# Kernel optimization log

Measured on AMD Instinct MI355X. Metric: run time of the kernel, lower is better.

Reference implementation:

```python
import jax, jax.numpy as jnp
import numpy as np

C = 256
CQK = C // 8  # 32

def setup_inputs() -> dict:
    key = jax.random.key(0)
    ks = jax.random.split(key, 8)
    B, W, H = 4, 64, 64
    s = 0.02
    x = jax.random.normal(ks[0], (B, C, W, H), dtype=jnp.float32)
    Wq = jax.random.normal(ks[1], (CQK, C), dtype=jnp.float32) * s
    bq = jnp.zeros((CQK,), dtype=jnp.float32)
    Wk = jax.random.normal(ks[2], (CQK, C), dtype=jnp.float32) * s
    bk = jnp.zeros((CQK,), dtype=jnp.float32)
    Wv = jax.random.normal(ks[3], (C, C), dtype=jnp.float32) * s
    bv = jnp.zeros((C,), dtype=jnp.float32)
    gamma = jnp.ones((1,), dtype=jnp.float32)  # nonzero so attention path matters
    return {"x": x, "Wq": Wq, "bq": bq, "Wk": Wk, "bk": bk, "Wv": Wv, "bv": bv, "gamma": gamma}

def reference(x, Wq, bq, Wk, bk, Wv, bv, gamma):
    B, Cc, W, H = x.shape
    N = W * H
    xf = x.reshape(B, Cc, N)  # B, C, N (flattened spatial)
    # 1x1 convs == channel-wise linear maps
    q = jnp.einsum('dc,bcn->bnd', Wq, xf) + bq[None, None, :]   # B, N, CQK
    k = jnp.einsum('dc,bcn->bdn', Wk, xf) + bk[None, :, None]   # B, CQK, N
    v = jnp.einsum('dc,bcn->bdn', Wv, xf) + bv[None, :, None]   # B, C, N
    energy = jnp.einsum('bnd,bdm->bnm', q, k)                   # B, N, N (unscaled)
    attention = jax.nn.softmax(energy, axis=-1)
    # out[:, :, i] = sum_j v[:, :, j] * attention[i, j]
    out = jnp.einsum('bdm,bnm->bdn', v, attention)              # B, C, N
    out = out.reshape(B, Cc, W, H)
    return gamma[0] * out + x
```

## Files before the change

kernel.cpp:

```cpp
#include <hip/hip_runtime.h>


#define CB  256
#define DQK 32
#define NN  4096
#define NB  4

typedef __attribute__((ext_vector_type(8))) short  short8;
typedef __attribute__((ext_vector_type(4))) float  f32x4;
typedef __attribute__((ext_vector_type(4))) unsigned short ushort4v;

__device__ inline unsigned short f2bf(float f) {
    union { float f; unsigned u; } cv; cv.f = f;
    unsigned u = cv.u;
    u += 0x7fffu + ((u >> 16) & 1u);
    return (unsigned short)(u >> 16);
}

__device__ inline float fast_exp2(float x) {
    float r;
    asm("v_exp_f32 %0, %1" : "=v"(r) : "v"(x));
    return r;
}

__device__ inline void gl16(const unsigned short* g, unsigned short* l) {
    __builtin_amdgcn_global_load_lds(
        (const __attribute__((address_space(1))) unsigned int*)g,
        (__attribute__((address_space(3))) unsigned int*)l, 16, 0, 0);
}

__device__ inline float bcast_row(const float* s, int lane) {
    int n = lane & 15;
    int src = (n >> 2) << 4;
    float b0 = __shfl(s[0], src, 64);
    float b1 = __shfl(s[1], src, 64);
    float b2 = __shfl(s[2], src, 64);
    float b3 = __shfl(s[3], src, 64);
    float r01 = (n & 1) ? b1 : b0;
    float r23 = (n & 1) ? b3 : b2;
    return (n & 2) ? r23 : r01;
}

__global__ __launch_bounds__(256) void proj_mfma(
    const float* __restrict__ x,
    const float* __restrict__ Wq, const float* __restrict__ bq,
    const float* __restrict__ Wk, const float* __restrict__ bk,
    const float* __restrict__ Wv, const float* __restrict__ bv,
    unsigned short* __restrict__ qo,
    unsigned short* __restrict__ ko,
    unsigned short* __restrict__ vo)
{
    __shared__ unsigned short ws[64 * 256];
    __shared__ unsigned short xs[64 * 256];

    const int bid = blockIdx.x;
    const int nb  = bid / 5;
    const int mg  = bid % 5;
    const int b   = nb >> 6;
    const int n0  = (nb & 63) << 6;
    const int t   = threadIdx.x;
    const int w   = t >> 6;
    const int lane = t & 63;

    {
        const int row = t >> 2;
        const int q4  = t & 3;
        const float* wsrc;
        if (mg < 4) wsrc = Wv + (size_t)(mg * 64 + row) * CB;
        else        wsrc = (row < 32) ? (Wq + (size_t)row * CB)
                                      : (Wk + (size_t)(row - 32) * CB);
        #pragma unroll
        for (int o = 0; o < 8; ++o) {
            int c = q4 * 64 + o * 8;
            f32x4 a0 = *(const f32x4*)(wsrc + c);
            f32x4 a1 = *(const f32x4*)(wsrc + c + 4);
            short8 pk;
            pk[0]=(short)f2bf(a0[0]); pk[1]=(short)f2bf(a0[1]);
            pk[2]=(short)f2bf(a0[2]); pk[3]=(short)f2bf(a0[3]);
            pk[4]=(short)f2bf(a1[0]); pk[5]=(short)f2bf(a1[1]);
            pk[6]=(short)f2bf(a1[2]); pk[7]=(short)f2bf(a1[3]);
            *(short8*)((char*)ws + row * 512 + ((c * 2) ^ ((row & 7) << 4))) = pk;
        }
    }
    {
        const float* xb = x + (size_t)b * CB * NN + n0;
        #pragma unroll
        for (int o = 0; o < 8; ++o) {
            int c0 = w * 64 + o * 8;
            float tf[8];
            #pragma unroll
            for (int i = 0; i < 8; ++i)
                tf[i] = xb[(size_t)(c0 + i) * NN + lane];
            short8 pk;
            #pragma unroll
            for (int i = 0; i < 8; ++i) pk[i] = (short)f2bf(tf[i]);
            *(short8*)((char*)xs + lane * 512 + ((c0 * 2) ^ ((lane & 7) << 4))) = pk;
        }
    }
    __syncthreads();

    const int l15 = lane & 15, l4 = lane >> 4;
    f32x4 acc[4];
    #pragma unroll
    for (int i = 0; i < 4; ++i) acc[i] = (f32x4){0.f, 0.f, 0.f, 0.f};

    #pragma unroll
    for (int kk = 0; kk < 8; ++kk) {
        int kb = kk * 64 + l4 * 16;
        int mrow = w * 16 + l15;
        short8 af = *(const short8*)((char*)ws + mrow * 512 + (kb ^ ((l15 & 7) << 4)));
        #pragma unroll
        for (int nf = 0; nf < 4; ++nf) {
            int n = nf * 16 + l15;
            short8 bfr = *(const short8*)((char*)xs + n * 512 + (kb ^ ((l15 & 7) << 4)));
            acc[nf] = __builtin_amdgcn_mfma_f32_16x16x32_bf16(af, bfr, acc[nf], 0, 0, 0);
        }
    }

    if (mg < 4) {
        #pragma unroll
        for (int nf = 0; nf < 4; ++nf) {
            #pragma unroll
            for (int r = 0; r < 4; ++r) {
                int m = mg * 64 + w * 16 + l4 * 4 + r;
                float val = acc[nf][r] + bv[m];
                vo[((size_t)b * CB + m) * NN + n0 + nf * 16 + l15] = f2bf(val);
            }
        }
    } else {
        const int dl = w * 16 + l4 * 4;
        #pragma unroll
        for (int nf = 0; nf < 4; ++nf) {
            size_t n = (size_t)b * NN + n0 + nf * 16 + l15;
            ushort4v pk;
            if (dl < 32) {
                #pragma unroll
                for (int r = 0; r < 4; ++r) pk[r] = f2bf(acc[nf][r] + bq[dl + r]);
                *(ushort4v*)(qo + n * DQK + dl) = pk;
            } else {
                #pragma unroll
                for (int r = 0; r < 4; ++r) pk[r] = f2bf(acc[nf][r] + bk[dl - 32 + r]);
                *(ushort4v*)(ko + n * DQK + dl - 32) = pk;
            }
        }
    }
}

__global__ __launch_bounds__(512, 4) void attn_kernel(
    const unsigned short* __restrict__ q,
    const unsigned short* __restrict__ k,
    const unsigned short* __restrict__ v,
    const float* __restrict__ x,
    const float* __restrict__ gamma,
    float* __restrict__ out)
{
    __shared__ unsigned short ksl[64 * 32];
    __shared__ unsigned short vsl[128 * 64];
    __shared__ unsigned short plds[8][1024];

    const int bid = blockIdx.x;
    const int swz = (bid & 7) * 64 + (bid >> 3);
    const int dh = swz & 1;
    const int nt = (swz >> 1) & 63;
    const int b  = swz >> 7;
    const int n0 = nt << 6;
    const int d0 = dh << 7;

    const int t    = threadIdx.x;
    const int w    = t >> 6;
    const int lane = t & 63;
    const int l15  = lane & 15;
    const int l4   = lane >> 4;
    const int qg   = w & 3;
    const int dsub = w >> 2;

    const unsigned short* qb = q + ((size_t)b * NN + n0 + qg * 16) * DQK;
    short8 qf = *(const short8*)(qb + (size_t)l15 * DQK + l4 * 8);

    f32x4 acc[4];
    #pragma unroll
    for (int i = 0; i < 4; ++i) acc[i] = (f32x4){0.f, 0.f, 0.f, 0.f};
    float psum[4] = {0.f, 0.f, 0.f, 0.f};

    const unsigned short* kb = k + (size_t)b * NN * DQK;
    const unsigned short* vb = v + (size_t)b * CB * NN;
    unsigned short* myp = plds[w];
    const float L2E = 1.44269504088896f;
    const f32x4 zero4 = {0.f, 0.f, 0.f, 0.f};

    const int krow = (w << 4) + (lane >> 2);
    const int kso  = (lane & 3) ^ ((lane >> 2) & 3);
    const int vso  = (lane & 7) ^ (lane >> 3);
    const int vrow0 = (w << 4) + (lane >> 3);
    const int vrow1 = vrow0 + 8;

    for (int m0 = 0; m0 < NN; m0 += 64) {
        __syncthreads();
        if (w < 4)
            gl16(kb + (size_t)(m0 + krow) * DQK + kso * 8, &ksl[w * 512]);
        gl16(vb + (size_t)(d0 + vrow0) * NN + m0 + vso * 8, &vsl[(w * 2 + 0) * 512]);
        gl16(vb + (size_t)(d0 + vrow1) * NN + m0 + vso * 8, &vsl[(w * 2 + 1) * 512]);
        asm volatile("s_waitcnt vmcnt(0)" ::: "memory");
        __syncthreads();

        f32x4 sf[4];
        #pragma unroll
        for (int mt = 0; mt < 4; ++mt) {
            int row  = mt * 16 + l15;
            int slot = l4 ^ (l15 & 3);
            short8 kf = *(const short8*)(&ksl[row * 32 + slot * 8]);
            sf[mt] = __builtin_amdgcn_mfma_f32_16x16x32_bf16(qf, kf, zero4, 0, 0, 0);
        }

        f32x4 pvv[4];
        #pragma unroll
        for (int r = 0; r < 4; ++r) {
            float p0 = fast_exp2(sf[0][r] * L2E);
            float p1 = fast_exp2(sf[1][r] * L2E);
            float p2 = fast_exp2(sf[2][r] * L2E);
            float p3 = fast_exp2(sf[3][r] * L2E);
            pvv[0][r] = p0; pvv[1][r] = p1; pvv[2][r] = p2; pvv[3][r] = p3;
            psum[r] += (p0 + p1) + (p2 + p3);
        }

        #pragma unroll
        for (int mt = 0; mt < 4; ++mt) {
            #pragma unroll
            for (int r = 0; r < 4; ++r) {
                int row = l4 * 4 + r;
                int col = mt * 16 + l15;
                int off = row * 128 + ((col * 2) ^ ((row & 7) << 4));
                myp[off >> 1] = f2bf(pvv[mt][r]);
            }
        }
        asm volatile("s_waitcnt lgkmcnt(0)" ::: "memory");
        __builtin_amdgcn_sched_barrier(0);

        short8 pb0, pb1;
        {
            int base = l15 * 128;
            int sw   = (l15 & 7) << 4;
            pb0 = *(const short8*)(myp + ((base + ((l4 * 16)      ^ sw)) >> 1));
            pb1 = *(const short8*)(myp + ((base + ((64 + l4 * 16) ^ sw)) >> 1));
        }

        #pragma unroll
        for (int dt = 0; dt < 4; ++dt) {
            int row = dsub * 64 + dt * 16 + l15;
            int s0  = (l4)     ^ (l15 & 7);
            int s1  = (4 + l4) ^ (l15 & 7);
            short8 vf0 = *(const short8*)(&vsl[row * 64 + s0 * 8]);
            short8 vf1 = *(const short8*)(&vsl[row * 64 + s1 * 8]);
            acc[dt] = __builtin_amdgcn_mfma_f32_16x16x32_bf16(vf0, pb0, acc[dt], 0, 0, 0);
            acc[dt] = __builtin_amdgcn_mfma_f32_16x16x32_bf16(vf1, pb1, acc[dt], 0, 0, 0);
        }
    }

    float runs[4];
    #pragma unroll
    for (int r = 0; r < 4; ++r) {
        float s = psum[r];
        s += __shfl_xor(s, 1); s += __shfl_xor(s, 2);
        s += __shfl_xor(s, 4); s += __shfl_xor(s, 8);
        runs[r] = s;
    }

    float rs  = bcast_row(runs, lane);
    float inv = 1.0f / rs;
    float g   = gamma[0];
    const size_t xoff = ((size_t)b * CB + d0 + dsub * 64) * NN + n0 + qg * 16;
    const float* xb = x + xoff;
    float*       ob = out + xoff;
    #pragma unroll
    for (int dt = 0; dt < 4; ++dt) {
        #pragma unroll
        for (int r = 0; r < 4; ++r) {
            size_t o = (size_t)(dt * 16 + l4 * 4 + r) * NN + l15;
            ob[o] = g * acc[dt][r] * inv + xb[o];
        }
    }
}

extern "C" void kernel_launch(void* const* d_in, const int* in_sizes, int n_in,
                              void* d_out, int out_size, void* d_ws, size_t ws_size,
                              hipStream_t stream) {
    const float* x     = (const float*)d_in[0];
    const float* Wq    = (const float*)d_in[1];
    const float* bq    = (const float*)d_in[2];
    const float* Wk    = (const float*)d_in[3];
    const float* bk    = (const float*)d_in[4];
    const float* Wv    = (const float*)d_in[5];
    const float* bv    = (const float*)d_in[6];
    const float* gamma = (const float*)d_in[7];
    float* out = (float*)d_out;

    unsigned short* qs = (unsigned short*)d_ws;
    unsigned short* ks = qs + (size_t)NB * NN * DQK;
    unsigned short* vs = ks + (size_t)NB * NN * DQK;

    proj_mfma<<<5 * NB * (NN / 64), 256, 0, stream>>>(x, Wq, bq, Wk, bk, Wv, bv, qs, ks, vs);
    attn_kernel<<<NB * (NN / 64) * 2, 512, 0, stream>>>(qs, ks, vs, x, gamma, out);
}
```

Baseline: 188.2 us.

## Double-buffer K/V tiles and fold log2e scale into Q projection

Attention kernel now stages K and V tiles into two LDS buffers so the next tile's global loads overlap the current tile's QK, softmax and PV MFMAs, with one barrier per iteration. The QK MFMA operands are swapped so scores come out transposed, which allows packed bf16 conversion and vectorized P stores, and reduces the final row-sum to two shuffles. The log2(e) factor is folded into Wq/bq in the projection kernel to remove a multiply per exp. This doubles K/V LDS usage, which may lower occupancy.

```diff
diff --git a/kernel.cpp b/kernel.cpp
--- a/kernel.cpp
+++ b/kernel.cpp
@@ -9,6 +9,9 @@
 typedef __attribute__((ext_vector_type(8))) short  short8;
 typedef __attribute__((ext_vector_type(4))) float  f32x4;
 typedef __attribute__((ext_vector_type(4))) unsigned short ushort4v;
+typedef __attribute__((ext_vector_type(2))) unsigned int   uint2v;
+
+#define L2E 1.44269504088896f
 
 __device__ inline unsigned short f2bf(float f) {
     union { float f; unsigned u; } cv; cv.f = f;
@@ -23,22 +26,16 @@
     return r;
 }
 
+__device__ inline unsigned int cvtpk(float lo, float hi) {
+    unsigned int r;
+    asm("v_cvt_pk_bf16_f32 %0, %1, %2" : "=v"(r) : "v"(lo), "v"(hi));
+    return r;
+}
+
 __device__ inline void gl16(const unsigned short* g, unsigned short* l) {
     __builtin_amdgcn_global_load_lds(
         (const __attribute__((address_space(1))) unsigned int*)g,
         (__attribute__((address_space(3))) unsigned int*)l, 16, 0, 0);
-}
-
-__device__ inline float bcast_row(const float* s, int lane) {
-    int n = lane & 15;
-    int src = (n >> 2) << 4;
-    float b0 = __shfl(s[0], src, 64);
-    float b1 = __shfl(s[1], src, 64);
-    float b2 = __shfl(s[2], src, 64);
-    float b3 = __shfl(s[3], src, 64);
-    float r01 = (n & 1) ? b1 : b0;
-    float r23 = (n & 1) ? b3 : b2;
-    return (n & 2) ? r23 : r01;
 }
 
 __global__ __launch_bounds__(256) void proj_mfma(
@@ -66,19 +63,20 @@
         const int row = t >> 2;
         const int q4  = t & 3;
         const float* wsrc;
+        float scale = 1.0f;
         if (mg < 4) wsrc = Wv + (size_t)(mg * 64 + row) * CB;
-        else        wsrc = (row < 32) ? (Wq + (size_t)row * CB)
-                                      : (Wk + (size_t)(row - 32) * CB);
+        else if (row < 32) { wsrc = Wq + (size_t)row * CB; scale = L2E; }
+        else               wsrc = Wk + (size_t)(row - 32) * CB;
         #pragma unroll
         for (int o = 0; o < 8; ++o) {
             int c = q4 * 64 + o * 8;
             f32x4 a0 = *(const f32x4*)(wsrc + c);
             f32x4 a1 = *(const f32x4*)(wsrc + c + 4);
             short8 pk;
-            pk[0]=(short)f2bf(a0[0]); pk[1]=(short)f2bf(a0[1]);
-            pk[2]=(short)f2bf(a0[2]); pk[3]=(short)f2bf(a0[3]);
-            pk[4]=(short)f2bf(a1[0]); pk[5]=(short)f2bf(a1[1]);
-            pk[6]=(short)f2bf(a1[2]); pk[7]=(short)f2bf(a1[3]);
+            pk[0]=(short)f2bf(a0[0]*scale); pk[1]=(short)f2bf(a0[1]*scale);
+            pk[2]=(short)f2bf(a0[2]*scale); pk[3]=(short)f2bf(a0[3]*scale);
+            pk[4]=(short)f2bf(a1[0]*scale); pk[5]=(short)f2bf(a1[1]*scale);
+            pk[6]=(short)f2bf(a1[2]*scale); pk[7]=(short)f2bf(a1[3]*scale);
             *(short8*)((char*)ws + row * 512 + ((c * 2) ^ ((row & 7) << 4))) = pk;
         }
     }
@@ -135,7 +133,7 @@
             ushort4v pk;
             if (dl < 32) {
                 #pragma unroll
-                for (int r = 0; r < 4; ++r) pk[r] = f2bf(acc[nf][r] + bq[dl + r]);
+                for (int r = 0; r < 4; ++r) pk[r] = f2bf(acc[nf][r] + bq[dl + r] * L2E);
                 *(ushort4v*)(qo + n * DQK + dl) = pk;
             } else {
                 #pragma unroll
@@ -154,8 +152,8 @@
     const float* __restrict__ gamma,
     float* __restrict__ out)
 {
-    __shared__ unsigned short ksl[64 * 32];
-    __shared__ unsigned short vsl[128 * 64];
+    __shared__ unsigned short ksl[2][64 * 32];
+    __shared__ unsigned short vsl[2][128 * 64];
     __shared__ unsigned short plds[8][1024];
 
     const int bid = blockIdx.x;
@@ -180,58 +178,67 @@
     f32x4 acc[4];
     #pragma unroll
     for (int i = 0; i < 4; ++i) acc[i] = (f32x4){0.f, 0.f, 0.f, 0.f};
-    float psum[4] = {0.f, 0.f, 0.f, 0.f};
+    float psum = 0.f;
 
     const unsigned short* kb = k + (size_t)b * NN * DQK;
     const unsigned short* vb = v + (size_t)b * CB * NN;
     unsigned short* myp = plds[w];
-    const float L2E = 1.44269504088896f;
     const f32x4 zero4 = {0.f, 0.f, 0.f, 0.f};
 
     const int krow = (w << 4) + (lane >> 2);
-    const int kso  = (lane & 3) ^ ((lane >> 2) & 3);
+    const int kso  = (lane & 3) ^ ((lane >> 2) & 3) ^ ((lane >> 4) & 3);
     const int vso  = (lane & 7) ^ (lane >> 3);
     const int vrow0 = (w << 4) + (lane >> 3);
     const int vrow1 = vrow0 + 8;
 
-    for (int m0 = 0; m0 < NN; m0 += 64) {
-        __syncthreads();
-        if (w < 4)
-            gl16(kb + (size_t)(m0 + krow) * DQK + kso * 8, &ksl[w * 512]);
-        gl16(vb + (size_t)(d0 + vrow0) * NN + m0 + vso * 8, &vsl[(w * 2 + 0) * 512]);
-        gl16(vb + (size_t)(d0 + vrow1) * NN + m0 + vso * 8, &vsl[(w * 2 + 1) * 512]);
-        asm volatile("s_waitcnt vmcnt(0)" ::: "memory");
-        __syncthreads();
+    const int kslot = (l4 ^ (l15 & 3) ^ ((l15 >> 2) & 3)) * 8;
+    const int vs0 = ((l4)     ^ (l15 & 7)) * 8;
+    const int vs1 = ((l4 + 4) ^ (l15 & 7)) * 8;
+    const int psw = (l15 & 7) << 4;
+
+    #define STAGE(buf, m0)                                                        \
+        do {                                                                      \
+            if (w < 4)                                                            \
+                gl16(kb + (size_t)((m0) + krow) * DQK + kso * 8, &ksl[buf][w * 512]); \
+            gl16(vb + (size_t)(d0 + vrow0) * NN + (m0) + vso * 8,                 \
+                 &vsl[buf][(w * 2 + 0) * 512]);                                   \
+            gl16(vb + (size_t)(d0 + vrow1) * NN + (m0) + vso * 8,                 \
+                 &vsl[buf][(w * 2 + 1) * 512]);                                   \
+        } while (0)
+
+    STAGE(0, 0);
+    __syncthreads();
+
+    for (int it = 0; it < 64; ++it) {
+        const int cur = it & 1;
+        if (it < 63) STAGE(cur ^ 1, (it + 1) * 64);
+
+        const unsigned short* kc = ksl[cur];
+        const unsigned short* vc = vsl[cur];
 
         f32x4 sf[4];
         #pragma unroll
         for (int mt = 0; mt < 4; ++mt) {
-            int row  = mt * 16 + l15;
-            int slot = l4 ^ (l15 & 3);
-            short8 kf = *(const short8*)(&ksl[row * 32 + slot * 8]);
-            sf[mt] = __builtin_amdgcn_mfma_f32_16x16x32_bf16(qf, kf, zero4, 0, 0, 0);
-        }
-
-        f32x4 pvv[4];
-        #pragma unroll
-        for (int r = 0; r < 4; ++r) {
-            float p0 = fast_exp2(sf[0][r] * L2E);
-            float p1 = fast_exp2(sf[1][r] * L2E);
-            float p2 = fast_exp2(sf[2][r] * L2E);
-            float p3 = fast_exp2(sf[3][r] * L2E);
-            pvv[0][r] = p0; pvv[1][r] = p1; pvv[2][r] = p2; pvv[3][r] = p3;
-            psum[r] += (p0 + p1) + (p2 + p3);
-        }
-
+            short8 kf = *(const short8*)(&kc[(mt * 16 + l15) * 32 + kslot]);
+            sf[mt] = __builtin_amdgcn_mfma_f32_16x16x32_bf16(kf, qf, zero4, 0, 0, 0);
+        }
+
+        unsigned int pw[4][2];
         #pragma unroll
         for (int mt = 0; mt < 4; ++mt) {
-            #pragma unroll
-            for (int r = 0; r < 4; ++r) {
-                int row = l4 * 4 + r;
-                int col = mt * 16 + l15;
-                int off = row * 128 + ((col * 2) ^ ((row & 7) << 4));
-                myp[off >> 1] = f2bf(pvv[mt][r]);
-            }
+            float p0 = fast_exp2(sf[mt][0]);
+            float p1 = fast_exp2(sf[mt][1]);
+            float p2 = fast_exp2(sf[mt][2]);
+            float p3 = fast_exp2(sf[mt][3]);
+            psum += (p0 + p1) + (p2 + p3);
+            pw[mt][0] = cvtpk(p0, p1);
+            pw[mt][1] = cvtpk(p2, p3);
+        }
+
+        #pragma unroll
+        for (int mt = 0; mt < 4; ++mt) {
+            int off = l15 * 128 + ((mt * 32 + l4 * 8) ^ psw);
+            *(uint2v*)((char*)myp + off) = (uint2v){pw[mt][0], pw[mt][1]};
         }
         asm volatile("s_waitcnt lgkmcnt(0)" ::: "memory");
         __builtin_amdgcn_sched_barrier(0);
@@ -239,35 +246,27 @@
         short8 pb0, pb1;
         {
             int base = l15 * 128;
-            int sw   = (l15 & 7) << 4;
-            pb0 = *(const short8*)(myp + ((base + ((l4 * 16)      ^ sw)) >> 1));
-            pb1 = *(const short8*)(myp + ((base + ((64 + l4 * 16) ^ sw)) >> 1));
+            pb0 = *(const short8*)(myp + ((base + ((l4 * 16)      ^ psw)) >> 1));
+            pb1 = *(const short8*)(myp + ((base + ((64 + l4 * 16) ^ psw)) >> 1));
         }
 
         #pragma unroll
         for (int dt = 0; dt < 4; ++dt) {
-            int row = dsub * 64 + dt * 16 + l15;
-            int s0  = (l4)     ^ (l15 & 7);
-            int s1  = (4 + l4) ^ (l15 & 7);
-            short8 vf0 = *(const short8*)(&vsl[row * 64 + s0 * 8]);
-            short8 vf1 = *(const short8*)(&vsl[row * 64 + s1 * 8]);
+            int rb = (dsub * 64 + dt * 16 + l15) * 64;
+            short8 vf0 = *(const short8*)(&vc[rb + vs0]);
+            short8 vf1 = *(const short8*)(&vc[rb + vs1]);
             acc[dt] = __builtin_amdgcn_mfma_f32_16x16x32_bf16(vf0, pb0, acc[dt], 0, 0, 0);
             acc[dt] = __builtin_amdgcn_mfma_f32_16x16x32_bf16(vf1, pb1, acc[dt], 0, 0, 0);
         }
-    }
-
-    float runs[4];
-    #pragma unroll
-    for (int r = 0; r < 4; ++r) {
-        float s = psum[r];
-        s += __shfl_xor(s, 1); s += __shfl_xor(s, 2);
-        s += __shfl_xor(s, 4); s += __shfl_xor(s, 8);
-        runs[r] = s;
-    }
-
-    float rs  = bcast_row(runs, lane);
-    float inv = 1.0f / rs;
+
+        __syncthreads();
+    }
+
+    psum += __shfl_xor(psum, 16);
+    psum += __shfl_xor(psum, 32);
+    float inv = 1.0f / psum;
     float g   = gamma[0];
+
     const size_t xoff = ((size_t)b * CB + d0 + dsub * 64) * NN + n0 + qg * 16;
     const float* xb = x + xoff;
     float*       ob = out + xoff;
@@ -279,6 +278,7 @@
             ob[o] = g * acc[dt][r] * inv + xb[o];
         }
     }
+    #undef STAGE
 }
 
 extern "C" void kernel_launch(void* const* d_in, const int* in_sizes, int n_in,
```

Result: faster. 178.8 us (-5.0%).
